# Kernel tuning notes

Hardware: AMD Instinct MI355X
Metric: run time of the kernel (lower is better)

## Reference

```python
import jax, jax.numpy as jnp
import numpy as np
import math

B, S, H, D = 1, 2048, 32, 128  # batch, local_seq (one ring block), num_heads, head_dim


def setup_inputs() -> dict:
    key = jax.random.key(0)
    kq, kk, kv = jax.random.split(key, 3)
    return {
        "query": jax.random.normal(kq, (B, S, H, D), dtype=jnp.float32),
        "key": jax.random.normal(kk, (B, S, H, D), dtype=jnp.float32),
        "value": jax.random.normal(kv, (B, S, H, D), dtype=jnp.float32),
    }


def reference(query, key, value):
    # RingAttention with world_size=1: a single ring step where q_block_idx == kv_block_idx,
    # i.e. standard causal attention on the local block. The online-softmax update from the
    # initial (output=0, lse=-inf) accumulator is the identity, so it is omitted.
    b, s, h, d = query.shape
    scale = 1.0 / math.sqrt(d)
    # [b, h, q, k] scores
    scores = jnp.einsum("bqhd,bkhd->bhqk", query, key) * scale
    causal = jnp.triu(jnp.ones((s, s), dtype=bool), k=1)  # True above diagonal -> masked
    scores = jnp.where(causal[None, None, :, :], -jnp.inf, scores)
    probs = jax.nn.softmax(scores, axis=-1)
    out = jnp.einsum("bhqk,bkhd->bqhd", probs, value)
    return out
```

## Files before the change

kernel.cpp:

```cpp
#include <hip/hip_runtime.h>
#include <hip/hip_bf16.h>
#include <stdint.h>

#define SEQ   2048
#define NHEAD 32
#define HDIM  128
#define RS    (NHEAD * HDIM)
#define KVBLK 64
#define QBLK  128
#define NTILES (SEQ / KVBLK)
#define TILE_BYTES 16384

typedef float  f32x16 __attribute__((ext_vector_type(16)));
typedef __bf16 bf16x8 __attribute__((ext_vector_type(8)));
typedef uint32_t u32;

__device__ __forceinline__ unsigned short f2bf(float f) {
  unsigned u = __builtin_bit_cast(unsigned, f);
  u += 0x7fffu + ((u >> 16) & 1u);
  return (unsigned short)(u >> 16);
}

__device__ __forceinline__ u32 packbf(float a, float b) {
  __bf16 x = (__bf16)a, y = (__bf16)b;
  unsigned short ux = __builtin_bit_cast(unsigned short, x);
  unsigned short uy = __builtin_bit_cast(unsigned short, y);
  return (u32)ux | ((u32)uy << 16);
}

__device__ __forceinline__ void gld16(const void* g, void* l) {
  __builtin_amdgcn_global_load_lds(
      (const __attribute__((address_space(1))) unsigned int*)g,
      (__attribute__((address_space(3))) unsigned int*)l, 16, 0, 0);
}

__global__ __launch_bounds__(256) void prepass_kernel(
    const float* __restrict__ K, const float* __restrict__ V,
    char* __restrict__ wsK, char* __restrict__ wsV) {
  const int tid = threadIdx.x;
  const int t   = blockIdx.x & (NTILES - 1);
  const int h   = blockIdx.x >> 5;
  const int kv0 = t * KVBLK;
  char* kd = wsK + (size_t)(h * NTILES + t) * TILE_BYTES;
  char* vd = wsV + (size_t)(h * NTILES + t) * TILE_BYTES;

  {
    const int c  = tid & 15;
    const int kr = tid >> 4;
#pragma unroll
    for (int ki = 0; ki < 4; ++ki) {
      const int kk = kr + ki * 16;
      const float* kp = K + (size_t)(kv0 + kk) * RS + h * HDIM + c * 8;
      float4 x0 = *(const float4*)kp;
      float4 x1 = *(const float4*)(kp + 4);
      uint32_t u0 = f2bf(x0.x) | ((uint32_t)f2bf(x0.y) << 16);
      uint32_t u1 = f2bf(x0.z) | ((uint32_t)f2bf(x0.w) << 16);
      uint32_t u2 = f2bf(x1.x) | ((uint32_t)f2bf(x1.y) << 16);
      uint32_t u3 = f2bf(x1.z) | ((uint32_t)f2bf(x1.w) << 16);
      const uint32_t byte = (uint32_t)(kk * 256) + (((uint32_t)(c * 16)) ^ (uint32_t)((kk & 15) << 4));
      *(uint4*)(kd + byte) = make_uint4(u0, u1, u2, u3);
    }
  }
  {
    const int d0  = (tid & 31) * 4;
    const int kk0 = (tid >> 5) * 8;
    float vv[8][4];
#pragma unroll
    for (int r = 0; r < 8; ++r) {
      const float* vp = V + (size_t)(kv0 + kk0 + r) * RS + h * HDIM + d0;
      float4 x = *(const float4*)vp;
      vv[r][0] = x.x; vv[r][1] = x.y; vv[r][2] = x.z; vv[r][3] = x.w;
    }
#pragma unroll
    for (int i = 0; i < 4; ++i) {
      const int d = d0 + i;
      uint32_t p0 = f2bf(vv[0][i]) | ((uint32_t)f2bf(vv[1][i]) << 16);
      uint32_t p1 = f2bf(vv[2][i]) | ((uint32_t)f2bf(vv[3][i]) << 16);
      uint32_t p2 = f2bf(vv[4][i]) | ((uint32_t)f2bf(vv[5][i]) << 16);
      uint32_t p3 = f2bf(vv[6][i]) | ((uint32_t)f2bf(vv[7][i]) << 16);
      const uint32_t byte = (uint32_t)(d * 128) + (((uint32_t)(kk0 * 2)) ^ (uint32_t)((d & 7) << 4));
      *(uint4*)(vd + byte) = make_uint4(p0, p1, p2, p3);
    }
  }
}

__global__ __launch_bounds__(256, 2) void fattn_main(
    const float* __restrict__ Q, const char* __restrict__ wsK,
    const char* __restrict__ wsV, float* __restrict__ O) {
  const int tid  = threadIdx.x;
  const int w    = tid >> 6;
  const int lane = tid & 63;
  const int n    = lane & 31;
  const int hh   = lane >> 5;

  const int bid  = blockIdx.x;
  const int b2   = bid & 255;
  const int vid  = (b2 & 7) * 32 + (b2 >> 3);
  const int head = vid >> 3;
  const int jj   = vid & 7;
  const int qb   = (bid < 256) ? (15 - jj) : jj;
  const int q0   = qb * QBLK;
  const int ntile  = 2 * qb + 2;
  const int diag_t = 2 * qb + (w >> 1);

  __shared__ __align__(16) char smem[65536];
  auto Kbuf = [&](int b) { return smem + b * 32768; };
  auto Vbuf = [&](int b) { return smem + b * 32768 + 16384; };

  const float qscale = 0.088388347648318447f * 1.4426950408889634f;

  const int qrow = q0 + w * 32 + n;

  bf16x8 bq[8];
  {
    const float* qp = Q + (size_t)qrow * RS + head * HDIM + hh * 8;
#pragma unroll
    for (int ks = 0; ks < 8; ++ks) {
      float4 v0 = *(const float4*)(qp + ks * 16);
      float4 v1 = *(const float4*)(qp + ks * 16 + 4);
      bf16x8 a;
      a[0] = (__bf16)(v0.x * qscale); a[1] = (__bf16)(v0.y * qscale);
      a[2] = (__bf16)(v0.z * qscale); a[3] = (__bf16)(v0.w * qscale);
      a[4] = (__bf16)(v1.x * qscale); a[5] = (__bf16)(v1.y * qscale);
      a[6] = (__bf16)(v1.z * qscale); a[7] = (__bf16)(v1.w * qscale);
      bq[ks] = a;
    }
  }

  f32x16 accO[4];
#pragma unroll
  for (int i = 0; i < 4; ++i) accO[i] = (f32x16)(0.f);
  float m_run  = -1e30f;
  float l_part = 0.f;

  const char* kbase = wsK + (size_t)head * NTILES * TILE_BYTES;
  const char* vbase = wsV + (size_t)head * NTILES * TILE_BYTES;
  const bool  doK   = (w < 2);
  const char* sbase = doK ? kbase : vbase;
  const int   half  = (w & 1) * 8192;

  auto stage = [&](int buf, int t) {
    const char* src = sbase + (size_t)t * TILE_BYTES + half + lane * 16;
    char* dst = (doK ? Kbuf(buf) : Vbuf(buf)) + half;
#pragma unroll
    for (int i = 0; i < 8; ++i) gld16(src + i * 1024, dst + i * 1024);
  };

  stage(0, 0);
  asm volatile("s_waitcnt vmcnt(0)" ::: "memory");
  __builtin_amdgcn_sched_barrier(0);
  __syncthreads();

  for (int t = 0; t < ntile; ++t) {
    const int cur = t & 1;
    if (t + 1 < ntile) stage(cur ^ 1, t + 1);

    if (t <= diag_t) {
      const char* Kc = Kbuf(cur);
      const char* Vc = Vbuf(cur);

      f32x16 sc[2];
      __builtin_amdgcn_s_setprio(1);
#pragma unroll
      for (int kt = 0; kt < 2; ++kt) {
        f32x16 acc = (f32x16)(0.f);
        const int key = kt * 32 + n;
        const uint32_t rowb = (uint32_t)(key * 256);
        const uint32_t swz  = (uint32_t)((key & 15) << 4);
#pragma unroll
        for (int ks = 0; ks < 8; ++ks) {
          const uint32_t byte = rowb + (((uint32_t)(ks * 32 + hh * 16)) ^ swz);
          bf16x8 kf = *(const bf16x8*)(Kc + byte);
          acc = __builtin_amdgcn_mfma_f32_32x32x16_bf16(kf, bq[ks], acc, 0, 0, 0);
        }
        sc[kt] = acc;
      }
      __builtin_amdgcn_s_setprio(0);

      if (t == diag_t) {
        const int kv0 = t * KVBLK;
#pragma unroll
        for (int kt = 0; kt < 2; ++kt)
#pragma unroll
          for (int r = 0; r < 16; ++r) {
            const int keyg = kv0 + kt * 32 + (r & 3) + 8 * (r >> 2) + 4 * hh;
            if (keyg > qrow) sc[kt][r] = -1e30f;
          }
      }

      float mx = -1e30f;
#pragma unroll
      for (int kt = 0; kt < 2; ++kt)
#pragma unroll
        for (int r = 0; r < 16; ++r) mx = fmaxf(mx, sc[kt][r]);
      mx = fmaxf(mx, __shfl_xor(mx, 32, 64));

      if (__any(mx - m_run > 11.0f)) {
        const float mn = fmaxf(m_run, mx);
        const float al = exp2f(m_run - mn);
        m_run = mn;
        l_part *= al;
#pragma unroll
        for (int r = 0; r < 16; ++r) {
          const float ar = __shfl(al, (r & 3) + 8 * (r >> 2) + 4 * hh, 64);
#pragma unroll
          for (int nt = 0; nt < 4; ++nt) accO[nt][r] *= ar;
        }
      }

      float ls = 0.f;
#pragma unroll
      for (int kt = 0; kt < 2; ++kt)
#pragma unroll
        for (int r = 0; r < 16; ++r) {
          const float p = exp2f(sc[kt][r] - m_run);
          sc[kt][r] = p;
          ls += p;
        }
      l_part += ls;

      u32 ua[2][4], ub[2][4];
#pragma unroll
      for (int kt = 0; kt < 2; ++kt)
#pragma unroll
        for (int i = 0; i < 4; ++i) {
          ua[kt][i] = packbf(sc[kt][4 * i],     sc[kt][4 * i + 1]);
          ub[kt][i] = packbf(sc[kt][4 * i + 2], sc[kt][4 * i + 3]);
        }

      u32 ra[2][2], rb[2][2];
#pragma unroll
      for (int kt = 0; kt < 2; ++kt)
#pragma unroll
        for (int q = 0; q < 2; ++q) {
          ra[kt][q] = __shfl_xor(hh ? ua[kt][2 * q] : ua[kt][2 * q + 1], 32, 64);
          rb[kt][q] = __shfl_xor(hh ? ub[kt][2 * q] : ub[kt][2 * q + 1], 32, 64);
        }

      __builtin_amdgcn_s_setprio(1);
#pragma unroll
      for (int s = 0; s < 4; ++s) {
        const int kt = s >> 1, q = s & 1;
        u32 af32[4];
        af32[0] = hh ? ra[kt][q] : ua[kt][2 * q];
        af32[1] = hh ? rb[kt][q] : ub[kt][2 * q];
        af32[2] = hh ? ua[kt][2 * q + 1] : ra[kt][q];
        af32[3] = hh ? ub[kt][2 * q + 1] : rb[kt][q];
        bf16x8 af = __builtin_bit_cast(bf16x8, *(uint4*)af32);
#pragma unroll
        for (int nt = 0; nt < 4; ++nt) {
          const int d = nt * 32 + n;
          const uint32_t byte = (uint32_t)(d * 128) +
              (((uint32_t)(s * 32 + hh * 16)) ^ (uint32_t)((d & 7) << 4));
          bf16x8 vf = *(const bf16x8*)(Vc + byte);
          accO[nt] = __builtin_amdgcn_mfma_f32_32x32x16_bf16(af, vf, accO[nt], 0, 0, 0);
        }
      }
      __builtin_amdgcn_s_setprio(0);
    }

    asm volatile("s_waitcnt vmcnt(0) lgkmcnt(0)" ::: "memory");
    __builtin_amdgcn_sched_barrier(0);
    __syncthreads();
  }

  const float lf  = l_part + __shfl_xor(l_part, 32, 64);
  const float inv = 1.0f / lf;
  float* ob = O + (size_t)(q0 + w * 32) * RS + head * HDIM;
#pragma unroll
  for (int r = 0; r < 16; ++r) {
    const int m = (r & 3) + 8 * (r >> 2) + 4 * hh;
    const float im = __shfl(inv, m, 64);
#pragma unroll
    for (int nt = 0; nt < 4; ++nt)
      ob[(size_t)m * RS + nt * 32 + n] = accO[nt][r] * im;
  }
}

extern "C" void kernel_launch(void* const* d_in, const int* in_sizes, int n_in,
                              void* d_out, int out_size, void* d_ws, size_t ws_size,
                              hipStream_t stream) {
  const float* q = (const float*)d_in[0];
  const float* k = (const float*)d_in[1];
  const float* v = (const float*)d_in[2];
  float* o = (float*)d_out;
  char* wsK = (char*)d_ws;
  char* wsV = wsK + (size_t)NHEAD * NTILES * TILE_BYTES;
  hipLaunchKernelGGL(prepass_kernel, dim3(NHEAD * NTILES), dim3(256), 0, stream,
                     k, v, wsK, wsV);
  hipLaunchKernelGGL(fattn_main, dim3(512), dim3(256), 0, stream, q, wsK, wsV, o);
}
```

Before: 88.42 us.

## Pre-arrange K/V workspace tiles in MFMA fragment order for linear LDS reads

The prep kernel now writes K and V bf16 tiles in exact MFMA fragment order: each 1 KB chunk holds one ks/kt (or s/nt) fragment, and lane i sits at offset 16*i. The main kernel reads each fragment with a fixed per-lane base plus a compile-time immediate offset, which removes the per-load XOR swizzle arithmetic and should keep LDS reads conflict-free. The row max is also reduced as a tree instead of a serial chain. The cost is a more scattered write pattern in the prep kernel's global stores.

```diff
diff --git a/kernel.cpp b/kernel.cpp
--- a/kernel.cpp
+++ b/kernel.cpp
@@ -57,7 +57,8 @@
       uint32_t u1 = f2bf(x0.z) | ((uint32_t)f2bf(x0.w) << 16);
       uint32_t u2 = f2bf(x1.x) | ((uint32_t)f2bf(x1.y) << 16);
       uint32_t u3 = f2bf(x1.z) | ((uint32_t)f2bf(x1.w) << 16);
-      const uint32_t byte = (uint32_t)(kk * 256) + (((uint32_t)(c * 16)) ^ (uint32_t)((kk & 15) << 4));
+      const int kt = kk >> 5, nn = kk & 31, ks = c >> 1, hh = c & 1;
+      const uint32_t byte = (uint32_t)((kt * 8 + ks) * 1024 + (hh * 32 + nn) * 16);
       *(uint4*)(kd + byte) = make_uint4(u0, u1, u2, u3);
     }
   }
@@ -71,6 +72,7 @@
       float4 x = *(const float4*)vp;
       vv[r][0] = x.x; vv[r][1] = x.y; vv[r][2] = x.z; vv[r][3] = x.w;
     }
+    const int s = kk0 >> 4, hh = (kk0 >> 3) & 1;
 #pragma unroll
     for (int i = 0; i < 4; ++i) {
       const int d = d0 + i;
@@ -78,7 +80,8 @@
       uint32_t p1 = f2bf(vv[2][i]) | ((uint32_t)f2bf(vv[3][i]) << 16);
       uint32_t p2 = f2bf(vv[4][i]) | ((uint32_t)f2bf(vv[5][i]) << 16);
       uint32_t p3 = f2bf(vv[6][i]) | ((uint32_t)f2bf(vv[7][i]) << 16);
-      const uint32_t byte = (uint32_t)(d * 128) + (((uint32_t)(kk0 * 2)) ^ (uint32_t)((d & 7) << 4));
+      const int nt = d >> 5;
+      const uint32_t byte = (uint32_t)((s * 4 + nt) * 1024 + (hh * 32 + (d & 31)) * 16);
       *(uint4*)(vd + byte) = make_uint4(p0, p1, p2, p3);
     }
   }
@@ -108,7 +111,6 @@
   auto Vbuf = [&](int b) { return smem + b * 32768 + 16384; };
 
   const float qscale = 0.088388347648318447f * 1.4426950408889634f;
-
   const int qrow = q0 + w * 32 + n;
 
   bf16x8 bq[8];
@@ -151,26 +153,24 @@
   __builtin_amdgcn_sched_barrier(0);
   __syncthreads();
 
+  const int lofs = lane * 16;
+
   for (int t = 0; t < ntile; ++t) {
     const int cur = t & 1;
     if (t + 1 < ntile) stage(cur ^ 1, t + 1);
 
     if (t <= diag_t) {
-      const char* Kc = Kbuf(cur);
-      const char* Vc = Vbuf(cur);
+      const char* Kc = Kbuf(cur) + lofs;
+      const char* Vc = Vbuf(cur) + lofs;
 
       f32x16 sc[2];
       __builtin_amdgcn_s_setprio(1);
 #pragma unroll
       for (int kt = 0; kt < 2; ++kt) {
         f32x16 acc = (f32x16)(0.f);
-        const int key = kt * 32 + n;
-        const uint32_t rowb = (uint32_t)(key * 256);
-        const uint32_t swz  = (uint32_t)((key & 15) << 4);
 #pragma unroll
         for (int ks = 0; ks < 8; ++ks) {
-          const uint32_t byte = rowb + (((uint32_t)(ks * 32 + hh * 16)) ^ swz);
-          bf16x8 kf = *(const bf16x8*)(Kc + byte);
+          bf16x8 kf = *(const bf16x8*)(Kc + (kt * 8 + ks) * 1024);
           acc = __builtin_amdgcn_mfma_f32_32x32x16_bf16(kf, bq[ks], acc, 0, 0, 0);
         }
         sc[kt] = acc;
@@ -188,11 +188,14 @@
           }
       }
 
-      float mx = -1e30f;
-#pragma unroll
-      for (int kt = 0; kt < 2; ++kt)
-#pragma unroll
-        for (int r = 0; r < 16; ++r) mx = fmaxf(mx, sc[kt][r]);
+      float tm[16];
+#pragma unroll
+      for (int r = 0; r < 16; ++r) tm[r] = fmaxf(sc[0][r], sc[1][r]);
+#pragma unroll
+      for (int r = 0; r < 8; ++r) tm[r] = fmaxf(tm[r], tm[r + 8]);
+#pragma unroll
+      for (int r = 0; r < 4; ++r) tm[r] = fmaxf(tm[r], tm[r + 4]);
+      float mx = fmaxf(fmaxf(tm[0], tm[1]), fmaxf(tm[2], tm[3]));
       mx = fmaxf(mx, __shfl_xor(mx, 32, 64));
 
       if (__any(mx - m_run > 11.0f)) {
@@ -227,7 +230,6 @@
           ua[kt][i] = packbf(sc[kt][4 * i],     sc[kt][4 * i + 1]);
           ub[kt][i] = packbf(sc[kt][4 * i + 2], sc[kt][4 * i + 3]);
         }
-
       u32 ra[2][2], rb[2][2];
 #pragma unroll
       for (int kt = 0; kt < 2; ++kt)
@@ -249,10 +251,7 @@
         bf16x8 af = __builtin_bit_cast(bf16x8, *(uint4*)af32);
 #pragma unroll
         for (int nt = 0; nt < 4; ++nt) {
-          const int d = nt * 32 + n;
-          const uint32_t byte = (uint32_t)(d * 128) +
-              (((uint32_t)(s * 32 + hh * 16)) ^ (uint32_t)((d & 7) << 4));
-          bf16x8 vf = *(const bf16x8*)(Vc + byte);
+          bf16x8 vf = *(const bf16x8*)(Vc + (s * 4 + nt) * 1024);
           accO[nt] = __builtin_amdgcn_mfma_f32_32x32x16_bf16(af, vf, accO[nt], 0, 0, 0);
         }
       }
```

New measurement: 89.23 us. Within noise of the previous version (+0.9%).
